# Kernel tuning notes

Measured on AMD Instinct MI355X. Metric: run time of the kernel, lower is better.

Reference implementation:

```python
import jax, jax.numpy as jnp
import numpy as np

SCALE = 1.0 / 16.0      # spatial scale: image coords -> feature-map coords (stride-16 backbone)
OUT = 7                 # roi_pool_outsize
RATIO = 2               # sampling_ratio
NUM_CLASSES = 21
HID = 1024
SCORE_THRESH = 0.05
NMS_THRESH = 0.5
DET = 100               # detections_per_img
MIN_SIZE = 0.01
LOG_MAX = float(np.log(1000.0 / 16.0))  # standard bbox decode dw/dh clamp


def _bilinear(feat, ys, xs):
    # feat [C,H,W]; ys [Py], xs [Px] -> [C,Py,Px] (torchvision roi_align interpolation, aligned=False)
    C, H, W = feat.shape
    vy = (ys > -1.0) & (ys < H)
    vx = (xs > -1.0) & (xs < W)
    y = jnp.clip(ys, 0.0, H - 1.0)
    x = jnp.clip(xs, 0.0, W - 1.0)
    y0 = jnp.floor(y).astype(jnp.int32)
    x0 = jnp.floor(x).astype(jnp.int32)
    y1 = jnp.minimum(y0 + 1, H - 1)
    x1 = jnp.minimum(x0 + 1, W - 1)
    ly = (y - y0)[:, None]
    lx = (x - x0)[None, :]
    f00 = feat[:, y0[:, None], x0[None, :]]
    f01 = feat[:, y0[:, None], x1[None, :]]
    f10 = feat[:, y1[:, None], x0[None, :]]
    f11 = feat[:, y1[:, None], x1[None, :]]
    val = (f00 * (1.0 - ly) * (1.0 - lx) + f01 * (1.0 - ly) * lx
           + f10 * ly * (1.0 - lx) + f11 * ly * lx)
    return val * (vy[:, None] & vx[None, :])


def _roi_align(features, boxes, bidx):
    # features [N,C,H,W], boxes [R,4] (image coords), bidx [R] -> [R,C,OUT,OUT]
    N, C, H, W = features.shape
    b = boxes * SCALE
    rw = jnp.maximum(b[:, 2] - b[:, 0], 1.0)
    rh = jnp.maximum(b[:, 3] - b[:, 1], 1.0)
    bw = rw / OUT
    bh = rh / OUT
    # per-bin sample offsets: (ph + (i+0.5)/ratio) for ph in [0,OUT), i in [0,RATIO)
    g = (jnp.arange(OUT, dtype=jnp.float32)[:, None]
         + (jnp.arange(RATIO, dtype=jnp.float32)[None, :] + 0.5) / RATIO).reshape(-1)  # [OUT*RATIO]
    ys = b[:, 1][:, None] + g[None, :] * bh[:, None]  # [R, OUT*RATIO]
    xs = b[:, 0][:, None] + g[None, :] * bw[:, None]
    vals = jax.vmap(lambda i, yr, xr: _bilinear(features[i], yr, xr))(bidx, ys, xs)  # [R,C,P,P]
    R = boxes.shape[0]
    return vals.reshape(R, C, OUT, RATIO, OUT, RATIO).mean(axis=(3, 5))


def _decode(deltas, props):
    # deltas [R,K,4], props [R,4]; weights (10,10,5,5) as in the module
    pw = props[:, 2] - props[:, 0]
    ph = props[:, 3] - props[:, 1]
    pcx = props[:, 0] + 0.5 * pw
    pcy = props[:, 1] + 0.5 * ph
    dx = deltas[..., 0] / 10.0
    dy = deltas[..., 1] / 10.0
    dw = jnp.minimum(deltas[..., 2] / 5.0, LOG_MAX)
    dh = jnp.minimum(deltas[..., 3] / 5.0, LOG_MAX)
    cx = dx * pw[:, None] + pcx[:, None]
    cy = dy * ph[:, None] + pcy[:, None]
    w = jnp.exp(dw) * pw[:, None]
    h = jnp.exp(dh) * ph[:, None]
    return jnp.stack([cx - 0.5 * w, cy - 0.5 * h, cx + 0.5 * w, cy + 0.5 * h], axis=-1)


def _per_image(scores, boxes, img):
    # scores [S,K], boxes [S,K,4]. Drop background class, flatten, filter, class-aware NMS, top-DET.
    S, K = scores.shape
    sc = scores[:, 1:].reshape(-1)                 # [M]
    bx = boxes[:, 1:, :].reshape(-1, 4)            # [M,4]
    lb = jnp.broadcast_to(jnp.arange(1, K, dtype=jnp.int32)[None, :], (S, K - 1)).reshape(-1)
    wv = bx[:, 2] - bx[:, 0]
    hv = bx[:, 3] - bx[:, 1]
    valid = (sc > SCORE_THRESH) & (wv >= MIN_SIZE) & (hv >= MIN_SIZE)
    live0 = jnp.where(valid, sc, -1.0)
    # batched_nms via per-class coordinate offsets
    nb = bx + (lb.astype(bx.dtype) * (img + 1.0))[:, None]
    areas = (nb[:, 2] - nb[:, 0]) * (nb[:, 3] - nb[:, 1])

    def step(live, _):
        i = jnp.argmax(live)
        s = live[i]
        b = nb[i]
        xx1 = jnp.maximum(b[0], nb[:, 0])
        yy1 = jnp.maximum(b[1], nb[:, 1])
        xx2 = jnp.minimum(b[2], nb[:, 2])
        yy2 = jnp.minimum(b[3], nb[:, 3])
        inter = jnp.maximum(xx2 - xx1, 0.0) * jnp.maximum(yy2 - yy1, 0.0)
        area_i = (b[2] - b[0]) * (b[3] - b[1])
        iou = inter / (area_i + areas - inter + 1e-9)
        live = jnp.where(iou > NMS_THRESH, -1.0, live)  # also suppresses i itself (iou=1)
        return live, (i, s)

    _, (idxs, svals) = jax.lax.scan(step, live0, None, length=DET)
    keep = svals > SCORE_THRESH
    out_boxes = jnp.where(keep[:, None], bx[idxs], 0.0)
    out_scores = jnp.where(keep, svals, 0.0)
    out_labels = jnp.where(keep, lb[idxs], 0)
    return out_boxes, out_scores, out_labels


def _forward(features, proposals, w1, b1, w2, b2, wc, bc, wb, bb, image_size):
    N, C, H, W = features.shape
    S = proposals.shape[1]
    props = proposals.reshape(-1, 4)
    bidx = jnp.repeat(jnp.arange(N), S)
    feats = _roi_align(features, props, bidx)          # [R,C,7,7]
    x = feats.reshape(N * S, -1)                       # [R, C*49]
    h = jax.nn.relu(x @ w1 + b1)
    h = jax.nn.relu(h @ w2 + b2)
    cls = h @ wc + bc                                  # [R,K]
    deltas = (h @ wb + bb).reshape(N * S, NUM_CLASSES, 4)
    scores = jax.nn.softmax(cls, axis=-1)
    boxes = _decode(deltas, props)                     # [R,K,4]
    img = float(image_size)
    boxes = jnp.clip(boxes, 0.0, img)                  # square image -> clip both coords to [0,img]
    scores = scores.reshape(N, S, NUM_CLASSES)
    boxes = boxes.reshape(N, S, NUM_CLASSES, 4)
    return jax.vmap(lambda s, bx: _per_image(s, bx, img))(scores, boxes)


def setup_inputs() -> dict:
    key = jax.random.key(0)
    ks = jax.random.split(key, 12)
    N, S, C, H, W = 2, 512, 512, 50, 50
    IMG = 800
    features = jax.random.normal(ks[0], (N, C, H, W), jnp.float32)
    x1 = jax.random.uniform(ks[1], (N, S)) * (IMG - 80.0)
    y1 = jax.random.uniform(ks[2], (N, S)) * (IMG - 80.0)
    x2 = jnp.minimum(x1 + 16.0 + jax.random.uniform(ks[3], (N, S)) * 180.0, float(IMG))
    y2 = jnp.minimum(y1 + 16.0 + jax.random.uniform(ks[4], (N, S)) * 180.0, float(IMG))
    proposals = jnp.stack([x1, y1, x2, y2], axis=-1)
    D = C * OUT * OUT  # 25088
    w1 = jax.random.normal(ks[5], (D, HID), jnp.float32) * 0.01
    b1 = jnp.zeros((HID,), jnp.float32)
    w2 = jax.random.normal(ks[6], (HID, HID), jnp.float32) * 0.02
    b2 = jnp.zeros((HID,), jnp.float32)
    wc = jax.random.normal(ks[7], (HID, NUM_CLASSES), jnp.float32) * 0.05
    bc = jnp.zeros((NUM_CLASSES,), jnp.float32)
    wb = jax.random.normal(ks[8], (HID, NUM_CLASSES * 4), jnp.float32) * 0.02
    bb = jnp.zeros((NUM_CLASSES * 4,), jnp.float32)
    return {"features": features, "proposals": proposals, "w1": w1, "b1": b1,
            "w2": w2, "b2": b2, "wc": wc, "bc": bc, "wb": wb, "bb": bb,
            "image_size": IMG}


def reference(features, proposals, w1, b1, w2, b2, wc, bc, wb, bb, image_size):
    boxes, scores, labels = _forward(features, proposals, w1, b1, w2, b2, wc, bc, wb, bb, image_size)
    return boxes, scores, labels
```

## Files before the change

kernel.cpp:

```cpp
#include <hip/hip_runtime.h>
#include <cmath>

#define NIMG 2
#define SPROP 512
#define NROI 1024
#define CCH 512
#define FH 50
#define FW 50
#define K1 25088
#define HID 1024
#define NCLS 21
#define NDET 100
#define IMGSZ 800.0f
#define LOGMAX 4.135166556742356f
#define MCAND 10240
#define ZSPLIT 8
#define KCHUNK 3136
#define ZSPLIT2 8
#define KCHUNK2 128

typedef unsigned short u16;
typedef __attribute__((ext_vector_type(8))) short short8;
typedef __attribute__((ext_vector_type(4))) float f32x4;
typedef __attribute__((ext_vector_type(16))) float f32x16;

__device__ __forceinline__ u16 f2bf(float x) {
  unsigned int u = __float_as_uint(x);
  u += 0x7fffu + ((u >> 16) & 1u);
  return (u16)(u >> 16);
}
__device__ __forceinline__ float bf2f(u16 h) {
  return __uint_as_float(((unsigned int)h) << 16);
}

template <bool BF16OUT>
__global__ __launch_bounds__(256) void roi_kernel(
    const float* __restrict__ feat, const float* __restrict__ props,
    float* __restrict__ X, u16* __restrict__ Xhi, u16* __restrict__ Xlo) {
  const int r = blockIdx.x;
  const int n = r >> 9;
  const int tid = threadIdx.x;
  __shared__ float tile[32][256];
  __shared__ int sy0[14], sy1[14], sx0[14], sx1[14];
  __shared__ float sly[14], slx[14], svy[14], svx[14];

  const float p0 = props[r * 4 + 0] * 0.0625f;
  const float p1 = props[r * 4 + 1] * 0.0625f;
  const float p2 = props[r * 4 + 2] * 0.0625f;
  const float p3 = props[r * 4 + 3] * 0.0625f;
  const float bw = fmaxf(p2 - p0, 1.0f) / 7.0f;
  const float bh = fmaxf(p3 - p1, 1.0f) / 7.0f;

  if (tid < 14) {
    const int j = tid;
    const float g = (float)(j >> 1) + ((float)(j & 1) + 0.5f) * 0.5f;
    float y = p1 + g * bh;
    svy[j] = (y > -1.0f && y < (float)FH) ? 1.0f : 0.0f;
    float yc = fminf(fmaxf(y, 0.0f), (float)(FH - 1));
    int y0 = (int)floorf(yc);
    sy0[j] = y0; sy1[j] = min(y0 + 1, FH - 1); sly[j] = yc - (float)y0;
    float x = p0 + g * bw;
    svx[j] = (x > -1.0f && x < (float)FW) ? 1.0f : 0.0f;
    float xc = fminf(fmaxf(x, 0.0f), (float)(FW - 1));
    int x0 = (int)floorf(xc);
    sx0[j] = x0; sx1[j] = min(x0 + 1, FW - 1); slx[j] = xc - (float)x0;
  }
  __syncthreads();
  const int ymin = sy0[0], xmin = sx0[0];
  const float* fb = feat + (size_t)n * CCH * (FH * FW);

  for (int cc = 0; cc < 16; ++cc) {
    const int c0 = cc * 32;
#pragma unroll
    for (int e = 0; e < 32; ++e) {
      const int idx = tid + e * 256;
      const int c = idx >> 8, p = idx & 255;
      const int gy = min(ymin + (p >> 4), FH - 1);
      const int gx = min(xmin + (p & 15), FW - 1);
      tile[c][p] = fb[(size_t)(c0 + c) * (FH * FW) + gy * FW + gx];
    }
    __syncthreads();
#pragma unroll
    for (int e = 0; e < 7; ++e) {
      const int idx = tid + e * 256;
      if (idx < 1568) {
        const int c = idx / 49;
        const int s = idx - c * 49;
        const int oy = s / 7, ox = s - (s / 7) * 7;
        float acc = 0.0f;
#pragma unroll
        for (int sy = 0; sy < 2; ++sy) {
          const int yj = oy * 2 + sy;
          const int py0 = sy0[yj] - ymin, py1 = sy1[yj] - ymin;
          const float ly = sly[yj], vy = svy[yj];
#pragma unroll
          for (int sx = 0; sx < 2; ++sx) {
            const int xj = ox * 2 + sx;
            const int px0 = sx0[xj] - xmin, px1 = sx1[xj] - xmin;
            const float lx = slx[xj], vx = svx[xj];
            const float f00 = tile[c][py0 * 16 + px0];
            const float f01 = tile[c][py0 * 16 + px1];
            const float f10 = tile[c][py1 * 16 + px0];
            const float f11 = tile[c][py1 * 16 + px1];
            float v = f00 * (1.0f - ly) * (1.0f - lx) + f01 * (1.0f - ly) * lx +
                      f10 * ly * (1.0f - lx) + f11 * ly * lx;
            acc += v * (vy * vx);
          }
        }
        const float v = acc * 0.25f;
        const size_t k = (size_t)r * K1 + (size_t)(c0 + c) * 49 + s;
        if (BF16OUT) {
          const u16 h = f2bf(v);
          Xhi[k] = h;
          Xlo[k] = f2bf(v - bf2f(h));
        } else {
          X[k] = v;
        }
      }
    }
    __syncthreads();
  }
}

template <int KDIM>
__global__ __launch_bounds__(256) void convw_kernel(
    const float* __restrict__ w, u16* __restrict__ Wh, u16* __restrict__ Wl) {
  __shared__ u16 sh[64][65], sl[64][65];
  const int k0 = blockIdx.x * 64;
  const int n0 = blockIdx.y * 64;
  const int t = threadIdx.x;
#pragma unroll
  for (int e = 0; e < 16; ++e) {
    const int idx = t + e * 256;
    const int kl = idx >> 6, nl = idx & 63;
    const float v = w[(size_t)(k0 + kl) * HID + n0 + nl];
    const u16 h = f2bf(v);
    sh[kl][nl] = h;
    sl[kl][nl] = f2bf(v - bf2f(h));
  }
  __syncthreads();
#pragma unroll
  for (int e = 0; e < 16; ++e) {
    const int idx = t + e * 256;
    const int nl = idx >> 6, kl = idx & 63;
    Wh[(size_t)(n0 + nl) * KDIM + k0 + kl] = sh[kl][nl];
    Wl[(size_t)(n0 + nl) * KDIM + k0 + kl] = sl[kl][nl];
  }
}

template <int KS, int KCH, bool SWZ>
__global__ __launch_bounds__(512, 2) void gemm_mfma_split(
    const u16* __restrict__ Ahg, const u16* __restrict__ Alg,
    const u16* __restrict__ Bhg, const u16* __restrict__ Blg,
    float* __restrict__ CP) {
  __shared__ u16 Ah[128][32], Al[128][32], Bh[256][32], Bl[256][32];
  const int tid = threadIdx.x;
  const int lane = tid & 63;
  const int wv = tid >> 6;
  const int wm = (wv >> 2) << 6;
  const int wn = (wv & 3) << 6;

  int bx = blockIdx.x, by = blockIdx.y, bz = blockIdx.z;
  if (SWZ) {
    const int f = blockIdx.x + ((blockIdx.y + (blockIdx.z << 3)) << 2);
    bz = f & 7;
    const int u = f >> 3;
    bx = u & 3;
    by = u >> 2;
  }
  const int mT = by << 7;
  const int nT = bx << 8;
  const int kz = bz * KCH;
  const int kend = kz + KCH;

  const int sr = tid >> 2;
  const int sq = (tid & 3) << 3;
  const int scw = (((tid & 3) ^ ((sr >> 1) & 3)) << 3);
  const size_t aoff  = (size_t)(mT + sr) * KS + sq;
  const size_t b0off = (size_t)(nT + sr) * KS + sq;
  const size_t b1off = (size_t)(nT + sr + 128) * KS + sq;

  f32x16 acc[2][2];
#pragma unroll
  for (int i = 0; i < 2; ++i)
#pragma unroll
    for (int j = 0; j < 2; ++j)
#pragma unroll
      for (int e = 0; e < 16; ++e) acc[i][j][e] = 0.0f;

  const int fm = lane & 31;
  const int fh = lane >> 5;
  const int vswz = (fm >> 1) & 3;

  uint4 rA  = *(const uint4*)(Ahg + aoff + kz);
  uint4 rL  = *(const uint4*)(Alg + aoff + kz);
  uint4 rB0 = *(const uint4*)(Bhg + b0off + kz);
  uint4 rB1 = *(const uint4*)(Bhg + b1off + kz);
  uint4 rM0 = *(const uint4*)(Blg + b0off + kz);
  uint4 rM1 = *(const uint4*)(Blg + b1off + kz);
  uint4 sA  = *(const uint4*)(Ahg + aoff + kz + 32);
  uint4 sL  = *(const uint4*)(Alg + aoff + kz + 32);
  uint4 sB0 = *(const uint4*)(Bhg + b0off + kz + 32);
  uint4 sB1 = *(const uint4*)(Bhg + b1off + kz + 32);
  uint4 sM0 = *(const uint4*)(Blg + b0off + kz + 32);
  uint4 sM1 = *(const uint4*)(Blg + b1off + kz + 32);

  auto compute = [&]() {
#pragma unroll
    for (int kh = 0; kh < 2; ++kh) {
      const int cA = ((((kh << 1) | fh) ^ vswz) << 3);
      short8 fa_h[2], fa_l[2], fb_h[2], fb_l[2];
#pragma unroll
      for (int t = 0; t < 2; ++t) {
        fa_h[t] = *(const short8*)(&Ah[wm + t * 32 + fm][cA]);
        fa_l[t] = *(const short8*)(&Al[wm + t * 32 + fm][cA]);
        fb_h[t] = *(const short8*)(&Bh[wn + t * 32 + fm][cA]);
        fb_l[t] = *(const short8*)(&Bl[wn + t * 32 + fm][cA]);
      }
#pragma unroll
      for (int ti = 0; ti < 2; ++ti)
#pragma unroll
        for (int tj = 0; tj < 2; ++tj) {
          acc[ti][tj] = __builtin_amdgcn_mfma_f32_32x32x16_bf16(
              fa_h[ti], fb_h[tj], acc[ti][tj], 0, 0, 0);
          acc[ti][tj] = __builtin_amdgcn_mfma_f32_32x32x16_bf16(
              fa_h[ti], fb_l[tj], acc[ti][tj], 0, 0, 0);
          acc[ti][tj] = __builtin_amdgcn_mfma_f32_32x32x16_bf16(
              fa_l[ti], fb_h[tj], acc[ti][tj], 0, 0, 0);
        }
    }
  };

  for (int kb = kz; kb < kend; kb += 64) {
    *(uint4*)(&Ah[sr][scw]) = rA;
    *(uint4*)(&Al[sr][scw]) = rL;
    *(uint4*)(&Bh[sr][scw]) = rB0;
    *(uint4*)(&Bh[sr + 128][scw]) = rB1;
    *(uint4*)(&Bl[sr][scw]) = rM0;
    *(uint4*)(&Bl[sr + 128][scw]) = rM1;
    __syncthreads();
    const int kn1 = (kb + 64 < kend) ? kb + 64 : kz;
    rA  = *(const uint4*)(Ahg + aoff + kn1);
    rL  = *(const uint4*)(Alg + aoff + kn1);
    rB0 = *(const uint4*)(Bhg + b0off + kn1);
    rB1 = *(const uint4*)(Bhg + b1off + kn1);
    rM0 = *(const uint4*)(Blg + b0off + kn1);
    rM1 = *(const uint4*)(Blg + b1off + kn1);
    compute();
    __syncthreads();
    *(uint4*)(&Ah[sr][scw]) = sA;
    *(uint4*)(&Al[sr][scw]) = sL;
    *(uint4*)(&Bh[sr][scw]) = sB0;
    *(uint4*)(&Bh[sr + 128][scw]) = sB1;
    *(uint4*)(&Bl[sr][scw]) = sM0;
    *(uint4*)(&Bl[sr + 128][scw]) = sM1;
    __syncthreads();
    const int kn2 = (kb + 96 < kend) ? kb + 96 : kz;
    sA  = *(const uint4*)(Ahg + aoff + kn2);
    sL  = *(const uint4*)(Alg + aoff + kn2);
    sB0 = *(const uint4*)(Bhg + b0off + kn2);
    sB1 = *(const uint4*)(Bhg + b1off + kn2);
    sM0 = *(const uint4*)(Blg + b0off + kn2);
    sM1 = *(const uint4*)(Blg + b1off + kn2);
    compute();
    __syncthreads();
  }

  float* Cp = CP + (size_t)bz * ((size_t)NROI * HID);
  const int ccol = nT + wn + fm;
  const int rbase = mT + wm + (fh << 2);
#pragma unroll
  for (int ti = 0; ti < 2; ++ti)
#pragma unroll
    for (int tj = 0; tj < 2; ++tj)
#pragma unroll
      for (int rg = 0; rg < 16; ++rg) {
        const int row = rbase + ti * 32 + (rg & 3) + 8 * (rg >> 2);
        Cp[(size_t)row * HID + ccol + tj * 32] = acc[ti][tj][rg];
      }
}

__global__ __launch_bounds__(256) void gemm1_kernel(
    const float* __restrict__ A, const float* __restrict__ B,
    float* __restrict__ CP) {
  __shared__ float As[16][68];
  __shared__ float Bs[16][68];
  const int tid = threadIdx.x;
  const int mTile = blockIdx.y << 6;
  const int nTile = blockIdx.x << 6;
  const int k0 = blockIdx.z * KCHUNK;
  const int ty = tid >> 4, tx = tid & 15;
  const int ar = tid >> 2, ac = (tid & 3) << 2;
  const int br = tid >> 4, bcl = (tid & 15) << 2;
  float acc[4][4] = {};

  for (int kb = k0; kb < k0 + KCHUNK; kb += 16) {
    const float4 av = *(const float4*)(A + (size_t)(mTile + ar) * K1 + kb + ac);
    const float4 bv = *(const float4*)(B + (size_t)(kb + br) * HID + nTile + bcl);
    As[ac + 0][ar] = av.x; As[ac + 1][ar] = av.y;
    As[ac + 2][ar] = av.z; As[ac + 3][ar] = av.w;
    *(float4*)(&Bs[br][bcl]) = bv;
    __syncthreads();
#pragma unroll
    for (int kk = 0; kk < 16; ++kk) {
      const float4 a4 = *(const float4*)(&As[kk][ty << 2]);
      const float4 b4 = *(const float4*)(&Bs[kk][tx << 2]);
      const float aa[4] = {a4.x, a4.y, a4.z, a4.w};
      const float bb4[4] = {b4.x, b4.y, b4.z, b4.w};
#pragma unroll
      for (int i = 0; i < 4; ++i)
#pragma unroll
        for (int j = 0; j < 4; ++j)
          acc[i][j] = fmaf(aa[i], bb4[j], acc[i][j]);
    }
    __syncthreads();
  }
  float* Cp = CP + (size_t)blockIdx.z * (HID * NROI);
#pragma unroll
  for (int i = 0; i < 4; ++i) {
    *(float4*)(Cp + (size_t)(mTile + (ty << 2) + i) * HID + nTile + (tx << 2)) =
        make_float4(acc[i][0], acc[i][1], acc[i][2], acc[i][3]);
  }
}

__global__ __launch_bounds__(256) void bias_relu_bf16_kernel(
    const float* __restrict__ CP, const float* __restrict__ b1,
    u16* __restrict__ H1h, u16* __restrict__ H1l) {
  const int idx = blockIdx.x * 256 + threadIdx.x;
  float v = b1[idx & (HID - 1)];
#pragma unroll
  for (int z = 0; z < ZSPLIT; ++z) v += CP[(size_t)z * (HID * NROI) + idx];
  v = fmaxf(v, 0.0f);
  const u16 h = f2bf(v);
  H1h[idx] = h;
  H1l[idx] = f2bf(v - bf2f(h));
}

__global__ __launch_bounds__(256) void bias_relu_f32_kernel(
    const float* __restrict__ CP, const float* __restrict__ b1,
    float* __restrict__ H1) {
  const int idx = blockIdx.x * 256 + threadIdx.x;
  float v = b1[idx & (HID - 1)];
#pragma unroll
  for (int z = 0; z < ZSPLIT; ++z) v += CP[(size_t)z * (HID * NROI) + idx];
  H1[idx] = fmaxf(v, 0.0f);
}

__global__ __launch_bounds__(256) void bias_relu2_kernel(
    const float* __restrict__ CP2, const float* __restrict__ b2,
    float* __restrict__ H2) {
  const int idx = blockIdx.x * 256 + threadIdx.x;
  float v = b2[idx & (HID - 1)];
#pragma unroll
  for (int z = 0; z < ZSPLIT2; ++z) v += CP2[(size_t)z * (HID * NROI) + idx];
  H2[idx] = fmaxf(v, 0.0f);
}

__global__ __launch_bounds__(256) void gemm2_kernel(
    const float* __restrict__ A, const float* __restrict__ B,
    const float* __restrict__ bias, float* __restrict__ C) {
  __shared__ float As[16][68];
  __shared__ float Bs[16][68];
  const int tid = threadIdx.x;
  const int mTile = blockIdx.y << 6;
  const int nTile = blockIdx.x << 6;
  const int ty = tid >> 4, tx = tid & 15;
  const int ar = tid >> 2, ac = (tid & 3) << 2;
  const int br = tid >> 4, bcl = (tid & 15) << 2;
  float acc[4][4] = {};

  for (int kb = 0; kb < HID; kb += 16) {
    const float4 av = *(const float4*)(A + (size_t)(mTile + ar) * HID + kb + ac);
    const float4 bv = *(const float4*)(B + (size_t)(kb + br) * HID + nTile + bcl);
    As[ac + 0][ar] = av.x; As[ac + 1][ar] = av.y;
    As[ac + 2][ar] = av.z; As[ac + 3][ar] = av.w;
    *(float4*)(&Bs[br][bcl]) = bv;
    __syncthreads();
#pragma unroll
    for (int kk = 0; kk < 16; ++kk) {
      const float4 a4 = *(const float4*)(&As[kk][ty << 2]);
      const float4 b4 = *(const float4*)(&Bs[kk][tx << 2]);
      const float aa[4] = {a4.x, a4.y, a4.z, a4.w};
      const float bb4[4] = {b4.x, b4.y, b4.z, b4.w};
#pragma unroll
      for (int i = 0; i < 4; ++i)
#pragma unroll
        for (int j = 0; j < 4; ++j)
          acc[i][j] = fmaf(aa[i], bb4[j], acc[i][j]);
    }
    __syncthreads();
  }
#pragma unroll
  for (int i = 0; i < 4; ++i) {
#pragma unroll
    for (int j = 0; j < 4; ++j) {
      float v = acc[i][j] + bias[nTile + (tx << 2) + j];
      acc[i][j] = fmaxf(v, 0.0f);
    }
    *(float4*)(C + (size_t)(mTile + (ty << 2) + i) * HID + nTile + (tx << 2)) =
        make_float4(acc[i][0], acc[i][1], acc[i][2], acc[i][3]);
  }
}

__global__ __launch_bounds__(128) void heads_kernel(
    const float* __restrict__ H2m, const float* __restrict__ wc,
    const float* __restrict__ bc, const float* __restrict__ wb,
    const float* __restrict__ bb, const float* __restrict__ props,
    float* __restrict__ BX2, float* __restrict__ NB2,
    float* __restrict__ LV2) {
  const int r = blockIdx.x;
  const int tid = threadIdx.x;
  __shared__ float hrow[HID];
  __shared__ float vals[112];
  __shared__ float red[2];

  for (int i = tid; i < HID; i += 128) hrow[i] = H2m[(size_t)r * HID + i];
  __syncthreads();

  if (tid < 105) {
    float acc;
    if (tid < NCLS) {
      acc = bc[tid];
      for (int kk = 0; kk < HID; ++kk) acc = fmaf(hrow[kk], wc[kk * NCLS + tid], acc);
    } else {
      const int j = tid - NCLS;
      acc = bb[j];
      for (int kk = 0; kk < HID; ++kk) acc = fmaf(hrow[kk], wb[kk * (NCLS * 4) + j], acc);
    }
    vals[tid] = acc;
  }
  __syncthreads();

  if (tid == 0) {
    float m = vals[0];
    for (int k = 1; k < NCLS; ++k) m = fmaxf(m, vals[k]);
    float s = 0.0f;
    for (int k = 0; k < NCLS; ++k) s += expf(vals[k] - m);
    red[0] = m;
    red[1] = 1.0f / s;
  }
  __syncthreads();

  if (tid >= 1 && tid <= 20) {
    const int k = tid;
    const float prob = expf(vals[k] - red[0]) * red[1];

    const float px1 = props[r * 4 + 0], py1 = props[r * 4 + 1];
    const float px2 = props[r * 4 + 2], py2 = props[r * 4 + 3];
    const float pw = px2 - px1, ph = py2 - py1;
    const float pcx = px1 + 0.5f * pw, pcy = py1 + 0.5f * ph;

    const float dx = vals[NCLS + k * 4 + 0] / 10.0f;
    const float dy = vals[NCLS + k * 4 + 1] / 10.0f;
    const float dw = fminf(vals[NCLS + k * 4 + 2] / 5.0f, LOGMAX);
    const float dh = fminf(vals[NCLS + k * 4 + 3] / 5.0f, LOGMAX);

    const float cx = dx * pw + pcx, cy = dy * ph + pcy;
    const float w = expf(dw) * pw, h = expf(dh) * ph;
    float b0 = cx - 0.5f * w, b1c = cy - 0.5f * h;
    float b2 = cx + 0.5f * w, b3 = cy + 0.5f * h;
    b0 = fminf(fmaxf(b0, 0.0f), IMGSZ);
    b1c = fminf(fmaxf(b1c, 0.0f), IMGSZ);
    b2 = fminf(fmaxf(b2, 0.0f), IMGSZ);
    b3 = fminf(fmaxf(b3, 0.0f), IMGSZ);

    const float wv = b2 - b0, hv = b3 - b1c;
    const bool valid = (prob > 0.05f) && (wv >= 0.01f) && (hv >= 0.01f);

    const int n = r >> 9, s = r & 511;
    const int cand = (k - 1) * SPROP + s;
    const size_t bi = (size_t)n * MCAND + cand;
    const float off = (float)k * (IMGSZ + 1.0f);

    BX2[bi * 4 + 0] = b0; BX2[bi * 4 + 1] = b1c;
    BX2[bi * 4 + 2] = b2; BX2[bi * 4 + 3] = b3;
    NB2[bi * 4 + 0] = b0 + off; NB2[bi * 4 + 1] = b1c + off;
    NB2[bi * 4 + 2] = b2 + off; NB2[bi * 4 + 3] = b3 + off;
    LV2[bi] = valid ? prob : -1.0f;
  }
}

template <int CTRL>
__device__ __forceinline__ void red2(float& v, int& ix) {
  const float tv = __int_as_float(__builtin_amdgcn_update_dpp(
      (int)0xC0000000, __float_as_int(v), CTRL, 0xf, 0xf, false));
  const int ti = __builtin_amdgcn_update_dpp(0x7fffffff, ix, CTRL, 0xf, 0xf, false);
  if (tv > v || (tv == v && ti < ix)) { v = tv; ix = ti; }
}
__device__ __forceinline__ void wave_red2(float& v, int& ix) {
  red2<0x111>(v, ix);
  red2<0x112>(v, ix);
  red2<0x114>(v, ix);
  red2<0x118>(v, ix);
  red2<0x142>(v, ix);
  red2<0x143>(v, ix);
}

__global__ __launch_bounds__(64) void nms_class_kernel(
    const float* __restrict__ NB2, const float* __restrict__ LV2,
    float* __restrict__ ksg, int* __restrict__ kig, int* __restrict__ cntg) {
  const int bid = blockIdx.x;
  const int lane = threadIdx.x;
  __shared__ float4 lbox[SPROP];
  const size_t cb = (size_t)bid * SPROP;

  float lv[8], b0[8], b1[8], b2[8], b3[8], ar[8];
#pragma unroll
  for (int j = 0; j < 8; ++j) {
    const int s = lane + j * 64;
    lv[j] = LV2[cb + s];
    const float4 b = *(const float4*)(NB2 + (cb + s) * 4);
    b0[j] = b.x; b1[j] = b.y; b2[j] = b.z; b3[j] = b.w;
    ar[j] = (b.z - b.x) * (b.w - b.y);
    lbox[s] = b;
  }

  int cnt = 0;
  for (int d = 0; d < NDET; ++d) {
    float bv = -2.0f;
    int bix = 0x7fffffff;
#pragma unroll
    for (int j = 0; j < 8; ++j) {
      if (lv[j] > bv) { bv = lv[j]; bix = lane + j * 64; }
    }
    wave_red2(bv, bix);
    const float bv2 = __shfl(bv, 63);
    const int bix2 = __shfl(bix, 63);
    if (bv2 <= 0.05f) break;

    if (lane == 0) {
      ksg[bid * NDET + cnt] = bv2;
      kig[bid * NDET + cnt] = bix2;
    }
    ++cnt;

    const float4 wb = lbox[bix2];
    const float wa = (wb.z - wb.x) * (wb.w - wb.y);
#pragma unroll
    for (int j = 0; j < 8; ++j) {
      const float xx1 = fmaxf(wb.x, b0[j]);
      const float yy1 = fmaxf(wb.y, b1[j]);
      const float xx2 = fminf(wb.z, b2[j]);
      const float yy2 = fminf(wb.w, b3[j]);
      const float inter = fmaxf(xx2 - xx1, 0.0f) * fmaxf(yy2 - yy1, 0.0f);
      const float iou = inter / (wa + ar[j] - inter + 1e-9f);
      if (iou > 0.5f) lv[j] = -1.0f;
    }
  }
  if (lane == 0) cntg[bid] = cnt;
}

__global__ __launch_bounds__(1024) void nms_merge_kernel(
    const float* __restrict__ ksg, const int* __restrict__ kig,
    const int* __restrict__ cntg, const float* __restrict__ BX2,
    float* __restrict__ out) {
  const int n = blockIdx.x;
  const int tid = threadIdx.x;
  __shared__ int cbase[21];
  __shared__ unsigned long long keys[2000];
  __shared__ float ssc[2000];
  __shared__ int sfl[2000];
  __shared__ float svals[NDET];
  __shared__ int sflat[NDET];

  if (tid == 0) {
    int acc = 0;
    for (int c = 0; c < 20; ++c) { cbase[c] = acc; acc += cntg[n * 20 + c]; }
    cbase[20] = acc;
  }
  __syncthreads();
  const int T = cbase[20];

  for (int idx = tid; idx < 20 * NDET; idx += 1024) {
    const int c = idx / NDET, e = idx - (idx / NDET) * NDET;
    if (e < cntg[n * 20 + c]) {
      const int pos = cbase[c] + e;
      const float s = ksg[(n * 20 + c) * NDET + e];
      const int slot = kig[(n * 20 + c) * NDET + e];
      const int flat = slot * 20 + c;
      ssc[pos] = s;
      sfl[pos] = flat;
      keys[pos] = ((unsigned long long)__float_as_uint(s) << 32) |
                  (unsigned long long)(0xFFFFFFFFu - (unsigned)flat);
    }
  }
  __syncthreads();

  float msc[2]; int mfl[2]; unsigned long long mk[2]; int rank[2] = {0, 0};
  bool own[2];
#pragma unroll
  for (int e = 0; e < 2; ++e) {
    const int i = tid + e * 1024;
    own[e] = (i < T);
    if (own[e]) { mk[e] = keys[i]; msc[e] = ssc[i]; mfl[e] = sfl[i]; }
  }
  for (int i = 0; i < T; ++i) {
    const unsigned long long k = keys[i];
    if (own[0] && k > mk[0]) ++rank[0];
    if (own[1] && k > mk[1]) ++rank[1];
  }
#pragma unroll
  for (int e = 0; e < 2; ++e)
    if (own[e] && rank[e] < NDET) { svals[rank[e]] = msc[e]; sflat[rank[e]] = mfl[e]; }
  __syncthreads();

  if (tid < NDET) {
    const int m = (T < NDET) ? T : NDET;
    const bool keep = tid < m;
    float sv = 0.0f;
    float4 bx4 = make_float4(0.0f, 0.0f, 0.0f, 0.0f);
    float label = 0.0f;
    if (keep) {
      sv = svals[tid];
      const int flat = sflat[tid];
      const int c = flat % 20, s = flat / 20;
      bx4 = *(const float4*)(BX2 + ((size_t)(n * 20 + c) * SPROP + s) * 4);
      label = (float)(c + 1);
    }
    out[(n * NDET + tid) * 4 + 0] = bx4.x;
    out[(n * NDET + tid) * 4 + 1] = bx4.y;
    out[(n * NDET + tid) * 4 + 2] = bx4.z;
    out[(n * NDET + tid) * 4 + 3] = bx4.w;
    out[NIMG * NDET * 4 + n * NDET + tid] = sv;
    out[NIMG * NDET * 4 + NIMG * NDET + n * NDET + tid] = label;
  }
}

extern "C" void kernel_launch(void* const* d_in, const int* in_sizes, int n_in,
                              void* d_out, int out_size, void* d_ws, size_t ws_size,
                              hipStream_t stream) {
  const float* features  = (const float*)d_in[0];
  const float* proposals = (const float*)d_in[1];
  const float* w1 = (const float*)d_in[2];
  const float* b1 = (const float*)d_in[3];
  const float* w2 = (const float*)d_in[4];
  const float* b2 = (const float*)d_in[5];
  const float* wc = (const float*)d_in[6];
  const float* bc = (const float*)d_in[7];
  const float* wb = (const float*)d_in[8];
  const float* bb = (const float*)d_in[9];

  const size_t XE = (size_t)NROI * K1;
  const size_t WE = (size_t)K1 * HID;
  const size_t FLOATS_TAIL =
      (size_t)ZSPLIT * NROI * HID + 2 * (size_t)NROI * HID + (size_t)NIMG * MCAND * 10;
  const size_t NEED = (XE * 2 + WE * 2) * sizeof(u16) + FLOATS_TAIL * sizeof(float);

  if (ws_size >= NEED) {
    u16* Xhi = (u16*)d_ws;
    u16* Xlo = Xhi + XE;
    u16* Wh  = Xlo + XE;
    u16* Wl  = Wh + WE;
    float* CP  = (float*)(Wl + WE);
    float* CP2 = CP;
    float* H2  = CP + (size_t)ZSPLIT * NROI * HID;
    float* BX2 = H2 + (size_t)NROI * HID;
    float* NB2 = BX2 + (size_t)NIMG * MCAND * 4;
    float* LV2 = NB2 + (size_t)NIMG * MCAND * 4;
    float* ksg = LV2 + (size_t)NIMG * MCAND;
    int*   kig = (int*)(ksg + (size_t)NIMG * 20 * NDET);
    int*   cntg = kig + (size_t)NIMG * 20 * NDET;
    u16* H1h = Xhi;
    u16* H1l = Xhi + (size_t)NROI * HID;
    u16* W2h = Xlo;
    u16* W2l = Xlo + (size_t)HID * HID;

    convw_kernel<K1><<<dim3(K1 / 64, HID / 64), 256, 0, stream>>>(w1, Wh, Wl);
    roi_kernel<true><<<NROI, 256, 0, stream>>>(features, proposals, nullptr, Xhi, Xlo);
    gemm_mfma_split<K1, KCHUNK, true><<<dim3(4, 8, ZSPLIT), 512, 0, stream>>>(
        Xhi, Xlo, Wh, Wl, CP);
    bias_relu_bf16_kernel<<<(NROI * HID) / 256, 256, 0, stream>>>(CP, b1, H1h, H1l);
    convw_kernel<HID><<<dim3(HID / 64, HID / 64), 256, 0, stream>>>(w2, W2h, W2l);
    gemm_mfma_split<HID, KCHUNK2, true><<<dim3(4, 8, ZSPLIT2), 512, 0, stream>>>(
        H1h, H1l, W2h, W2l, CP2);
    bias_relu2_kernel<<<(NROI * HID) / 256, 256, 0, stream>>>(CP2, b2, H2);
    heads_kernel<<<NROI, 128, 0, stream>>>(H2, wc, bc, wb, bb, proposals,
                                           BX2, NB2, LV2);
    nms_class_kernel<<<NIMG * 20, 64, 0, stream>>>(NB2, LV2, ksg, kig, cntg);
    nms_merge_kernel<<<NIMG, 1024, 0, stream>>>(ksg, kig, cntg, BX2,
                                                (float*)d_out);
  } else {
    float* ws = (float*)d_ws;
    float* X   = ws;
    float* CP  = X + XE;
    float* H1  = CP + (size_t)ZSPLIT * NROI * HID;
    float* H2  = H1 + (size_t)NROI * HID;
    float* BX2 = H2 + (size_t)NROI * HID;
    float* NB2 = BX2 + (size_t)NIMG * MCAND * 4;
    float* LV2 = NB2 + (size_t)NIMG * MCAND * 4;
    float* ksg = LV2 + (size_t)NIMG * MCAND;
    int*   kig = (int*)(ksg + (size_t)NIMG * 20 * NDET);
    int*   cntg = kig + (size_t)NIMG * 20 * NDET;

    roi_kernel<false><<<NROI, 256, 0, stream>>>(features, proposals, X, nullptr, nullptr);
    gemm1_kernel<<<dim3(16, 16, ZSPLIT), 256, 0, stream>>>(X, w1, CP);
    bias_relu_f32_kernel<<<(NROI * HID) / 256, 256, 0, stream>>>(CP, b1, H1);
    gemm2_kernel<<<dim3(16, 16), 256, 0, stream>>>(H1, w2, b2, H2);
    heads_kernel<<<NROI, 128, 0, stream>>>(H2, wc, bc, wb, bb, proposals,
                                           BX2, NB2, LV2);
    nms_class_kernel<<<NIMG * 20, 64, 0, stream>>>(NB2, LV2, ksg, kig, cntg);
    nms_merge_kernel<<<NIMG, 1024, 0, stream>>>(ksg, kig, cntg, BX2,
                                                (float*)d_out);
  }
}
```

Before: 835.4 us.

## Prefetch ROI feature tiles into registers and pad shared tile layout

Restructures the ROI-align kernel so each thread loads the next 32-channel chunk of the feature window into registers while the current chunk is interpolated from shared memory. The shared tile is padded (row stride 17, channel stride 273) to reduce bank conflicts. Per-sample interpolation metadata is precomputed as packed float4 weights with validity and the 0.25 averaging folded in. The cost is more registers (32 prefetch floats), which may reduce occupancy, and the register path relies on the ROI window fitting 16x16.

```diff
diff --git a/kernel.cpp b/kernel.cpp
--- a/kernel.cpp
+++ b/kernel.cpp
@@ -40,9 +40,10 @@
   const int r = blockIdx.x;
   const int n = r >> 9;
   const int tid = threadIdx.x;
-  __shared__ float tile[32][256];
-  __shared__ int sy0[14], sy1[14], sx0[14], sx1[14];
-  __shared__ float sly[14], slx[14], svy[14], svx[14];
+  __shared__ float tile[32 * 273 + 16];
+  __shared__ float4 ymeta[14];
+  __shared__ float4 xmeta[14];
+  __shared__ int smin[2];
 
   const float p0 = props[r * 4 + 0] * 0.0625f;
   const float p1 = props[r * 4 + 1] * 0.0625f;
@@ -54,67 +55,103 @@
   if (tid < 14) {
     const int j = tid;
     const float g = (float)(j >> 1) + ((float)(j & 1) + 0.5f) * 0.5f;
-    float y = p1 + g * bh;
-    svy[j] = (y > -1.0f && y < (float)FH) ? 1.0f : 0.0f;
-    float yc = fminf(fmaxf(y, 0.0f), (float)(FH - 1));
-    int y0 = (int)floorf(yc);
-    sy0[j] = y0; sy1[j] = min(y0 + 1, FH - 1); sly[j] = yc - (float)y0;
-    float x = p0 + g * bw;
-    svx[j] = (x > -1.0f && x < (float)FW) ? 1.0f : 0.0f;
-    float xc = fminf(fmaxf(x, 0.0f), (float)(FW - 1));
-    int x0 = (int)floorf(xc);
-    sx0[j] = x0; sx1[j] = min(x0 + 1, FW - 1); slx[j] = xc - (float)x0;
+    const float y = p1 + g * bh;
+    const float vy = (y > -1.0f && y < (float)FH) ? 0.5f : 0.0f;
+    const float yc = fminf(fmaxf(y, 0.0f), (float)(FH - 1));
+    const int y0 = (int)floorf(yc);
+    const int y1 = min(y0 + 1, FH - 1);
+    const float ly = yc - (float)y0;
+    const float yc0 = fminf(fmaxf(p1 + 0.25f * bh, 0.0f), (float)(FH - 1));
+    const int ymin = (int)floorf(yc0);
+    float4 m;
+    m.x = __int_as_float((y0 - ymin) * 17);
+    m.y = __int_as_float((y1 - ymin) * 17);
+    m.z = (1.0f - ly) * vy;
+    m.w = ly * vy;
+    ymeta[j] = m;
+    if (j == 0) smin[0] = ymin;
+  } else if (tid >= 16 && tid < 30) {
+    const int j = tid - 16;
+    const float g = (float)(j >> 1) + ((float)(j & 1) + 0.5f) * 0.5f;
+    const float x = p0 + g * bw;
+    const float vx = (x > -1.0f && x < (float)FW) ? 0.5f : 0.0f;
+    const float xc = fminf(fmaxf(x, 0.0f), (float)(FW - 1));
+    const int x0 = (int)floorf(xc);
+    const int x1 = min(x0 + 1, FW - 1);
+    const float lx = xc - (float)x0;
+    const float xc0 = fminf(fmaxf(p0 + 0.25f * bw, 0.0f), (float)(FW - 1));
+    const int xmin = (int)floorf(xc0);
+    const float wx0 = (1.0f - lx) * vx;
+    const float wx1 = lx * vx;
+    const int d = x1 - x0;
+    float4 m;
+    m.x = __int_as_float(x0 - xmin);
+    m.y = wx0 + (d ? 0.0f : wx1);
+    m.z = d ? wx1 : 0.0f;
+    m.w = 0.0f;
+    xmeta[j] = m;
+    if (j == 0) smin[1] = xmin;
   }
   __syncthreads();
-  const int ymin = sy0[0], xmin = sx0[0];
+
+  const int ymin = smin[0], xmin = smin[1];
   const float* fb = feat + (size_t)n * CCH * (FH * FW);
+  const int gy = min(ymin + (tid >> 4), FH - 1);
+  const int gx = min(xmin + (tid & 15), FW - 1);
+  const int offp = gy * FW + gx;
+  const int wslot = (tid >> 4) * 17 + (tid & 15);
+  const int q = tid & 7;
+  const int c = tid >> 3;
+  const int cb = c * 273;
+
+  float pf[32];
+#pragma unroll
+  for (int e = 0; e < 32; ++e) pf[e] = fb[(size_t)e * (FH * FW) + offp];
 
   for (int cc = 0; cc < 16; ++cc) {
-    const int c0 = cc * 32;
-#pragma unroll
-    for (int e = 0; e < 32; ++e) {
-      const int idx = tid + e * 256;
-      const int c = idx >> 8, p = idx & 255;
-      const int gy = min(ymin + (p >> 4), FH - 1);
-      const int gx = min(xmin + (p & 15), FW - 1);
-      tile[c][p] = fb[(size_t)(c0 + c) * (FH * FW) + gy * FW + gx];
-    }
-    __syncthreads();
-#pragma unroll
-    for (int e = 0; e < 7; ++e) {
-      const int idx = tid + e * 256;
-      if (idx < 1568) {
-        const int c = idx / 49;
-        const int s = idx - c * 49;
-        const int oy = s / 7, ox = s - (s / 7) * 7;
+#pragma unroll
+    for (int e = 0; e < 32; ++e) tile[e * 273 + wslot] = pf[e];
+    __syncthreads();
+    if (cc < 15) {
+      const float* fb2 = fb + (size_t)(cc + 1) * 32 * (FH * FW);
+#pragma unroll
+      for (int e = 0; e < 32; ++e) pf[e] = fb2[(size_t)e * (FH * FW) + offp];
+    }
+#pragma unroll
+    for (int jj = 0; jj < 7; ++jj) {
+      const int s = q + (jj << 3);
+      if (s < 49) {
+        const int oy = s / 7;
+        const int ox = s - oy * 7;
+        const float4 ym0 = ymeta[2 * oy];
+        const float4 ym1 = ymeta[2 * oy + 1];
+        const float4 xm0 = xmeta[2 * ox];
+        const float4 xm1 = xmeta[2 * ox + 1];
         float acc = 0.0f;
 #pragma unroll
         for (int sy = 0; sy < 2; ++sy) {
-          const int yj = oy * 2 + sy;
-          const int py0 = sy0[yj] - ymin, py1 = sy1[yj] - ymin;
-          const float ly = sly[yj], vy = svy[yj];
+          const float4 ym = sy ? ym1 : ym0;
+          const int ro0 = cb + __float_as_int(ym.x);
+          const int ro1 = cb + __float_as_int(ym.y);
 #pragma unroll
           for (int sx = 0; sx < 2; ++sx) {
-            const int xj = ox * 2 + sx;
-            const int px0 = sx0[xj] - xmin, px1 = sx1[xj] - xmin;
-            const float lx = slx[xj], vx = svx[xj];
-            const float f00 = tile[c][py0 * 16 + px0];
-            const float f01 = tile[c][py0 * 16 + px1];
-            const float f10 = tile[c][py1 * 16 + px0];
-            const float f11 = tile[c][py1 * 16 + px1];
-            float v = f00 * (1.0f - ly) * (1.0f - lx) + f01 * (1.0f - ly) * lx +
-                      f10 * ly * (1.0f - lx) + f11 * ly * lx;
-            acc += v * (vy * vx);
+            const float4 xm = sx ? xm1 : xm0;
+            const int px = __float_as_int(xm.x);
+            const float a0 = tile[ro0 + px];
+            const float a1 = tile[ro0 + px + 1];
+            const float b0 = tile[ro1 + px];
+            const float b1 = tile[ro1 + px + 1];
+            acc += ym.z * (xm.y * a0 + xm.z * a1) +
+                   ym.w * (xm.y * b0 + xm.z * b1);
           }
         }
-        const float v = acc * 0.25f;
-        const size_t k = (size_t)r * K1 + (size_t)(c0 + c) * 49 + s;
+        const size_t k = (size_t)r * K1 + (size_t)(cc * 32 + c) * 49 + s;
         if (BF16OUT) {
-          const u16 h = f2bf(v);
+          const u16 h = f2bf(acc);
           Xhi[k] = h;
-          Xlo[k] = f2bf(v - bf2f(h));
+          Xlo[k] = f2bf(acc - bf2f(h));
         } else {
-          X[k] = v;
+          X[k] = acc;
         }
       }
     }
```

Result: faster. 792.9 us (-5.1%).
